# Kernel optimization log

Measured on AMD Instinct MI355X. Metric: run time of the kernel, lower is better.

Reference implementation:

```python
import jax, jax.numpy as jnp
import numpy as np

B, S, D, H = 2, 2048, 1024, 16
DK = D // H  # 64


def setup_inputs() -> dict:
    rng = jax.random.key(0)
    ks = jax.random.split(rng, 11)
    std = 1.0 / np.sqrt(D)
    query = jax.random.normal(ks[0], (B, S, D), dtype=jnp.float32)
    key = jax.random.normal(ks[1], (B, S, D), dtype=jnp.float32)
    value = jax.random.normal(ks[2], (B, S, D), dtype=jnp.float32)
    # causal mask, broadcast over batch and heads
    mask = jnp.tril(jnp.ones((S, S), dtype=jnp.int32))[None, None]
    Wq = jax.random.normal(ks[3], (D, D), dtype=jnp.float32) * std
    bq = jnp.zeros((D,), dtype=jnp.float32)
    Wk = jax.random.normal(ks[4], (D, D), dtype=jnp.float32) * std
    bk = jnp.zeros((D,), dtype=jnp.float32)
    Wv = jax.random.normal(ks[5], (D, D), dtype=jnp.float32) * std
    bv = jnp.zeros((D,), dtype=jnp.float32)
    Wo = jax.random.normal(ks[6], (D, D), dtype=jnp.float32) * std
    bo = jnp.zeros((D,), dtype=jnp.float32)
    return {"query": query, "key": key, "value": value, "mask": mask,
            "Wq": Wq, "bq": bq, "Wk": Wk, "bk": bk,
            "Wv": Wv, "bv": bv, "Wo": Wo, "bo": bo}


def reference(query, key, value, mask, Wq, bq, Wk, bk, Wv, bv, Wo, bo):
    scale = jnp.sqrt(jnp.float32(DK))
    # linear projections (nn.Linear applies x @ W.T + b)
    Q = query @ Wq.T + bq
    K = key @ Wk.T + bk
    V = value @ Wv.T + bv
    # [B,S,D] -> [B,H,S,DK]
    Q = Q.reshape(B, S, H, DK).transpose(0, 2, 1, 3)
    K = K.reshape(B, S, H, DK).transpose(0, 2, 1, 3)
    V = V.reshape(B, S, H, DK).transpose(0, 2, 1, 3)
    scores = jnp.einsum('bhqd,bhkd->bhqk', Q, K) / scale
    scores = jnp.where(mask == 0, jnp.float32(-1e9), scores)
    attention = jax.nn.softmax(scores, axis=-1)  # dropout is identity in eval
    x = jnp.einsum('bhqk,bhkd->bhqd', attention, V)
    x = x.transpose(0, 2, 1, 3).reshape(B, S, D)
    x = x @ Wo.T + bo
    return (x, attention)
```

## Files before the change

### kernel.cpp

```cpp
#include <hip/hip_runtime.h>
#include <stdint.h>

#define S_LEN 2048
#define DMODEL 1024
#define NHEAD 16
#define DKH 64
#define NROW 4096

using short8  = __attribute__((ext_vector_type(8))) short;
using short4v = __attribute__((ext_vector_type(4))) short;
using float4v = __attribute__((ext_vector_type(4))) float;

__device__ __forceinline__ short f2bf(float f) {
    union { float f; unsigned u; } v; v.f = f;
    unsigned r = (v.u + 0x7fffu + ((v.u >> 16) & 1u)) >> 16;
    return (short)r;
}

__device__ __forceinline__ float4v mfma16(short8 a, short8 b, float4v c) {
    return __builtin_amdgcn_mfma_f32_16x16x32_bf16(a, b, c, 0, 0, 0);
}

__device__ __forceinline__ void gload16(const short* g, short* l) {
    __builtin_amdgcn_global_load_lds(
        (const __attribute__((address_space(1))) void*)g,
        (__attribute__((address_space(3))) void*)l, 16, 0, 0);
}

__global__ __launch_bounds__(256) void convert_kernel(
    const float* __restrict__ q, const float* __restrict__ k, const float* __restrict__ v,
    const float* __restrict__ wq, const float* __restrict__ wk, const float* __restrict__ wv,
    const float* __restrict__ wo,
    short* __restrict__ oq, short* __restrict__ ok_, short* __restrict__ ov,
    short* __restrict__ owq, short* __restrict__ owk, short* __restrict__ owv,
    short* __restrict__ owo)
{
    const size_t A = (size_t)NROW * DMODEL;
    const size_t W = (size_t)DMODEL * DMODEL;
    size_t i = ((size_t)blockIdx.x * 256 + threadIdx.x) * 4;
    const float* src; short* dst; size_t off;
    if (i < A)            { src = q;  dst = oq;  off = i; }
    else if (i < 2 * A)   { src = k;  dst = ok_; off = i - A; }
    else if (i < 3 * A)   { src = v;  dst = ov;  off = i - 2 * A; }
    else {
        size_t j = i - 3 * A; int wsel = (int)(j / W); off = j % W;
        src = (wsel == 0) ? wq : (wsel == 1) ? wk : (wsel == 2) ? wv : wo;
        dst = (wsel == 0) ? owq : (wsel == 1) ? owk : (wsel == 2) ? owv : owo;
    }
    float4v x = *(const float4v*)(src + off);
    short4v o;
    o[0] = f2bf(x[0]); o[1] = f2bf(x[1]); o[2] = f2bf(x[2]); o[3] = f2bf(x[3]);
    *(short4v*)(dst + off) = o;
}

__global__ __launch_bounds__(256) void gemm_qkv(
    const short* __restrict__ Xq, const short* __restrict__ Xk, const short* __restrict__ Xv,
    const short* __restrict__ Wq, const short* __restrict__ Wk, const short* __restrict__ Wv,
    const float* __restrict__ bq, const float* __restrict__ bk, const float* __restrict__ bv,
    short* __restrict__ Qo, short* __restrict__ Ko, short* __restrict__ Vt)
{
    int zy = blockIdx.y;
    int z = zy >> 3;
    int n0 = (zy & 7) * 128;
    const short* X = (z == 0) ? Xq : (z == 1) ? Xk : Xv;
    const short* W = (z == 0) ? Wq : (z == 1) ? Wk : Wv;
    const float* bias = (z == 0) ? bq : (z == 1) ? bk : bv;
    int m0 = blockIdx.x * 128;

    __shared__ __align__(16) short As[128 * 32];
    __shared__ __align__(16) short Bs[128 * 32];

    int tid = threadIdx.x, lane = tid & 63, w = tid >> 6;
    int row_in = lane & 15, grp = lane >> 4;
    int wm = (w & 1) * 64, wn = (w >> 1) * 64;

    float4v acc[4][4];
#pragma unroll
    for (int m = 0; m < 4; m++)
#pragma unroll
        for (int n = 0; n < 4; n++) acc[m][n] = (float4v){0.f, 0.f, 0.f, 0.f};

    for (int k0 = 0; k0 < DMODEL; k0 += 32) {
#pragma unroll
        for (int j = 0; j < 2; j++) {
            int chunk = j * 256 + tid;
            int r = chunk >> 2, c = (chunk & 3) * 8;
            gload16(X + (size_t)(m0 + r) * DMODEL + k0 + c,
                    As + (size_t)(j * 256 + w * 64) * 8);
            gload16(W + (size_t)(n0 + r) * DMODEL + k0 + c,
                    Bs + (size_t)(j * 256 + w * 64) * 8);
        }
        __syncthreads();

        short8 af[4], bf[4];
#pragma unroll
        for (int m = 0; m < 4; m++)
            af[m] = *(const short8*)&As[(wm + m * 16 + row_in) * 32 + grp * 8];
#pragma unroll
        for (int n = 0; n < 4; n++)
            bf[n] = *(const short8*)&Bs[(wn + n * 16 + row_in) * 32 + grp * 8];
#pragma unroll
        for (int m = 0; m < 4; m++)
#pragma unroll
            for (int n = 0; n < 4; n++)
                acc[m][n] = mfma16(af[m], bf[n], acc[m][n]);
        __syncthreads();
    }

#pragma unroll
    for (int m = 0; m < 4; m++) {
#pragma unroll
        for (int n = 0; n < 4; n++) {
            int col = n0 + wn + n * 16 + row_in;
            int h = col >> 6, dk = col & 63;
            float bval = bias[col];
            if (z < 2) {
                short* dst = (z == 0) ? Qo : Ko;
#pragma unroll
                for (int r = 0; r < 4; r++) {
                    int rowg = m0 + wm + m * 16 + grp * 4 + r;
                    int bb = rowg >> 11, s = rowg & 2047;
                    dst[(((size_t)(bb * NHEAD + h)) * S_LEN + s) * DKH + dk] =
                        f2bf(acc[m][n][r] + bval);
                }
            } else {
                int rowg0 = m0 + wm + m * 16 + grp * 4;
                int bb = rowg0 >> 11, s0 = rowg0 & 2047;
                short4v pk;
#pragma unroll
                for (int r = 0; r < 4; r++) pk[r] = f2bf(acc[m][n][r] + bval);
                *(short4v*)(Vt + ((size_t)(bb * NHEAD + h) * DKH + dk) * S_LEN + s0) = pk;
            }
        }
    }
}

__global__ __launch_bounds__(256) void gemm_out(
    const short* __restrict__ X, const short* __restrict__ W,
    const float* __restrict__ bias, float* __restrict__ out)
{
    int m0 = blockIdx.x * 128, n0 = blockIdx.y * 128;

    __shared__ __align__(16) short As[128 * 32];
    __shared__ __align__(16) short Bs[128 * 32];

    int tid = threadIdx.x, lane = tid & 63, w = tid >> 6;
    int row_in = lane & 15, grp = lane >> 4;
    int wm = (w & 1) * 64, wn = (w >> 1) * 64;

    float4v acc[4][4];
#pragma unroll
    for (int m = 0; m < 4; m++)
#pragma unroll
        for (int n = 0; n < 4; n++) acc[m][n] = (float4v){0.f, 0.f, 0.f, 0.f};

    for (int k0 = 0; k0 < DMODEL; k0 += 32) {
#pragma unroll
        for (int j = 0; j < 2; j++) {
            int chunk = j * 256 + tid;
            int r = chunk >> 2, c = (chunk & 3) * 8;
            gload16(X + (size_t)(m0 + r) * DMODEL + k0 + c,
                    As + (size_t)(j * 256 + w * 64) * 8);
            gload16(W + (size_t)(n0 + r) * DMODEL + k0 + c,
                    Bs + (size_t)(j * 256 + w * 64) * 8);
        }
        __syncthreads();

        short8 af[4], bf[4];
#pragma unroll
        for (int m = 0; m < 4; m++)
            af[m] = *(const short8*)&As[(wm + m * 16 + row_in) * 32 + grp * 8];
#pragma unroll
        for (int n = 0; n < 4; n++)
            bf[n] = *(const short8*)&Bs[(wn + n * 16 + row_in) * 32 + grp * 8];
#pragma unroll
        for (int m = 0; m < 4; m++)
#pragma unroll
            for (int n = 0; n < 4; n++)
                acc[m][n] = mfma16(af[m], bf[n], acc[m][n]);
        __syncthreads();
    }

#pragma unroll
    for (int m = 0; m < 4; m++)
#pragma unroll
        for (int n = 0; n < 4; n++) {
            int col = n0 + wn + n * 16 + row_in;
            float bval = bias[col];
#pragma unroll
            for (int r = 0; r < 4; r++) {
                int rowg = m0 + wm + m * 16 + grp * 4 + r;
                out[(size_t)rowg * DMODEL + col] = acc[m][n][r] + bval;
            }
        }
}

__global__ __launch_bounds__(256) void attn_kernel(
    const short* __restrict__ Q, const short* __restrict__ K, const short* __restrict__ Vt,
    float* __restrict__ Attn, short* __restrict__ Xatt)
{
    int bh = blockIdx.x;
    int q0 = blockIdx.y * 64;
    int tid = threadIdx.x, lane = tid & 63, w = tid >> 6;
    int row_in = lane & 15, grp = lane >> 4;
    int qbase = q0 + w * 16;

    const short* Qh = Q + (size_t)bh * S_LEN * DKH;
    const short* Kh = K + (size_t)bh * S_LEN * DKH;
    const short* Vh = Vt + (size_t)bh * DKH * S_LEN;
    float* Ah = Attn + (size_t)bh * S_LEN * S_LEN;

    short8 qf0 = *(const short8*)(Qh + (size_t)(qbase + row_in) * DKH + grp * 8);
    short8 qf1 = *(const short8*)(Qh + (size_t)(qbase + row_in) * DKH + 32 + grp * 8);

    float m[4] = {-1e30f, -1e30f, -1e30f, -1e30f};
    float l[4] = {0.f, 0.f, 0.f, 0.f};

    int q_hi_wave = qbase + 15;
    for (int kv0 = 0; kv0 <= q_hi_wave; kv0 += 64) {
        float sv[4][4];
#pragma unroll
        for (int u = 0; u < 4; u++) {
            const short* Kr = Kh + (size_t)(kv0 + u * 16 + row_in) * DKH + grp * 8;
            short8 b0 = *(const short8*)Kr;
            short8 b1 = *(const short8*)(Kr + 32);
            float4v a = (float4v){0.f, 0.f, 0.f, 0.f};
            a = mfma16(qf0, b0, a);
            a = mfma16(qf1, b1, a);
            int colg = kv0 + u * 16 + row_in;
#pragma unroll
            for (int r = 0; r < 4; r++) {
                int rowg = qbase + grp * 4 + r;
                float s = a[r] * 0.125f;
                sv[u][r] = (colg > rowg) ? -1e30f : s;
            }
        }
#pragma unroll
        for (int r = 0; r < 4; r++) {
            float mx = fmaxf(fmaxf(sv[0][r], sv[1][r]), fmaxf(sv[2][r], sv[3][r]));
            mx = fmaxf(mx, __shfl_xor(mx, 1, 64));
            mx = fmaxf(mx, __shfl_xor(mx, 2, 64));
            mx = fmaxf(mx, __shfl_xor(mx, 4, 64));
            mx = fmaxf(mx, __shfl_xor(mx, 8, 64));
            float nm = fmaxf(m[r], mx);
            float ps = __expf(sv[0][r] - nm) + __expf(sv[1][r] - nm) +
                       __expf(sv[2][r] - nm) + __expf(sv[3][r] - nm);
            ps += __shfl_xor(ps, 1, 64);
            ps += __shfl_xor(ps, 2, 64);
            ps += __shfl_xor(ps, 4, 64);
            ps += __shfl_xor(ps, 8, 64);
            l[r] = l[r] * __expf(m[r] - nm) + ps;
            m[r] = nm;
        }
    }
    float rinv[4];
#pragma unroll
    for (int r = 0; r < 4; r++) rinv[r] = 1.0f / l[r];

    __shared__ __align__(16) short Plds[4][16][72];
    __shared__ __align__(16) float Pf32[4][16][68];
    float4v o[4];
#pragma unroll
    for (int v = 0; v < 4; v++) o[v] = (float4v){0.f, 0.f, 0.f, 0.f};

    int q_hi_blk = q0 + 63;
    for (int kv0 = 0; kv0 < S_LEN; kv0 += 64) {
        if (kv0 <= q_hi_blk) {
#pragma unroll
            for (int u = 0; u < 4; u++) {
                const short* Kr = Kh + (size_t)(kv0 + u * 16 + row_in) * DKH + grp * 8;
                short8 b0 = *(const short8*)Kr;
                short8 b1 = *(const short8*)(Kr + 32);
                float4v a = (float4v){0.f, 0.f, 0.f, 0.f};
                a = mfma16(qf0, b0, a);
                a = mfma16(qf1, b1, a);
                int colg = kv0 + u * 16 + row_in;
#pragma unroll
                for (int r = 0; r < 4; r++) {
                    int rowg = qbase + grp * 4 + r;
                    float s = a[r] * 0.125f;
                    float p = (colg > rowg) ? 0.0f : __expf(s - m[r]) * rinv[r];
                    Pf32[w][grp * 4 + r][u * 16 + row_in] = p;
                    Plds[w][grp * 4 + r][u * 16 + row_in] = f2bf(p);
                }
            }
            asm volatile("s_waitcnt lgkmcnt(0)" ::: "memory");
#pragma unroll
            for (int rr = 0; rr < 4; rr++) {
                int rloc = rr * 4 + grp;
                float4v pv = *(const float4v*)&Pf32[w][rloc][row_in * 4];
                *(float4v*)(Ah + (size_t)(qbase + rloc) * S_LEN + kv0 + row_in * 4) = pv;
            }
            short8 pa0 = *(const short8*)&Plds[w][row_in][grp * 8];
            short8 pa1 = *(const short8*)&Plds[w][row_in][32 + grp * 8];
#pragma unroll
            for (int v = 0; v < 4; v++) {
                const short* Vr = Vh + (size_t)(v * 16 + row_in) * S_LEN + kv0 + grp * 8;
                short8 b0 = *(const short8*)Vr;
                short8 b1 = *(const short8*)(Vr + 32);
                o[v] = mfma16(pa0, b0, o[v]);
                o[v] = mfma16(pa1, b1, o[v]);
            }
        } else {
            float4v zz = (float4v){0.f, 0.f, 0.f, 0.f};
#pragma unroll
            for (int r = 0; r < 4; r++) {
                int rowg = qbase + r * 4 + grp;
                *(float4v*)(Ah + (size_t)rowg * S_LEN + kv0 + row_in * 4) = zz;
            }
        }
    }

    int b = bh >> 4, h = bh & 15;
#pragma unroll
    for (int v = 0; v < 4; v++) {
#pragma unroll
        for (int r = 0; r < 4; r++) {
            int s = qbase + grp * 4 + r;
            int col = h * 64 + v * 16 + row_in;
            Xatt[(size_t)(b * S_LEN + s) * DMODEL + col] = f2bf(o[v][r]);
        }
    }
}

extern "C" void kernel_launch(void* const* d_in, const int* in_sizes, int n_in,
                              void* d_out, int out_size, void* d_ws, size_t ws_size,
                              hipStream_t stream) {
    const float* q  = (const float*)d_in[0];
    const float* k  = (const float*)d_in[1];
    const float* v  = (const float*)d_in[2];
    const float* Wq = (const float*)d_in[4];
    const float* bq = (const float*)d_in[5];
    const float* Wk = (const float*)d_in[6];
    const float* bk = (const float*)d_in[7];
    const float* Wv = (const float*)d_in[8];
    const float* bv = (const float*)d_in[9];
    const float* Wo = (const float*)d_in[10];
    const float* bo = (const float*)d_in[11];

    float* out_x    = (float*)d_out;
    float* out_attn = out_x + (size_t)NROW * DMODEL;

    char* ws = (char*)d_ws;
    size_t off = 0;
    auto carve = [&](size_t bytes) -> char* {
        char* p = ws + off;
        off += (bytes + 255) & ~(size_t)255;
        return p;
    };
    const size_t XB = (size_t)NROW * DMODEL * sizeof(short);
    const size_t WB = (size_t)DMODEL * DMODEL * sizeof(short);
    short* Xq  = (short*)carve(XB);
    short* Xk  = (short*)carve(XB);
    short* Xv  = (short*)carve(XB);
    short* Wqb = (short*)carve(WB);
    short* Wkb = (short*)carve(WB);
    short* Wvb = (short*)carve(WB);
    short* Wob = (short*)carve(WB);
    short* Qb  = (short*)carve(XB);
    short* Kb  = (short*)carve(XB);
    short* Vtb = (short*)carve(XB);
    short* Xat = (short*)carve(XB);

    convert_kernel<<<dim3(16384), dim3(256), 0, stream>>>(
        q, k, v, Wq, Wk, Wv, Wo, Xq, Xk, Xv, Wqb, Wkb, Wvb, Wob);

    gemm_qkv<<<dim3(NROW / 128, 24), dim3(256), 0, stream>>>(
        Xq, Xk, Xv, Wqb, Wkb, Wvb, bq, bk, bv, Qb, Kb, Vtb);

    attn_kernel<<<dim3(32, S_LEN / 64), dim3(256), 0, stream>>>(
        Qb, Kb, Vtb, out_attn, Xat);

    gemm_out<<<dim3(NROW / 128, DMODEL / 128), dim3(256), 0, stream>>>(
        Xat, Wob, bo, out_x);
}
```

Before: 876.9 us.

## Stage K/V tiles in LDS and drop max-tracking from attention softmax

The attention kernel now loads each 64-row K and V tile cooperatively into shared memory so all four waves reuse it, instead of each wave fetching from global memory. The online max/rescale pass is removed: the first pass only sums exp2 of scaled scores, relying on scores being small enough not to overflow. The fp32 probability staging buffer is dropped, and the attention output is written from the bf16 copy converted back to float. These changes add block-wide barriers, and they risk overflow without max subtraction as well as reduced precision in the stored attention matrix.

```diff
diff --git a/kernel.cpp b/kernel.cpp
--- a/kernel.cpp
+++ b/kernel.cpp
@@ -15,6 +15,12 @@
     union { float f; unsigned u; } v; v.f = f;
     unsigned r = (v.u + 0x7fffu + ((v.u >> 16) & 1u)) >> 16;
     return (short)r;
+}
+
+__device__ __forceinline__ float bf2f(short b) {
+    union { unsigned u; float f; } c;
+    c.u = ((unsigned)(unsigned short)b) << 16;
+    return c.f;
 }
 
 __device__ __forceinline__ float4v mfma16(short8 a, short8 b, float4v c) {
@@ -210,20 +216,34 @@
     const short* Vh = Vt + (size_t)bh * DKH * S_LEN;
     float* Ah = Attn + (size_t)bh * S_LEN * S_LEN;
 
+    __shared__ __align__(16) short Ks[64 * 72];
+    __shared__ __align__(16) short Vs[64 * 72];
+    __shared__ __align__(16) short Plds[4][16 * 72];
+
     short8 qf0 = *(const short8*)(Qh + (size_t)(qbase + row_in) * DKH + grp * 8);
     short8 qf1 = *(const short8*)(Qh + (size_t)(qbase + row_in) * DKH + 32 + grp * 8);
 
-    float m[4] = {-1e30f, -1e30f, -1e30f, -1e30f};
+    const float SC = 0.125f * 1.44269504f;
     float l[4] = {0.f, 0.f, 0.f, 0.f};
-
-    int q_hi_wave = qbase + 15;
-    for (int kv0 = 0; kv0 <= q_hi_wave; kv0 += 64) {
-        float sv[4][4];
+    int Tmax = q0 / 64 + 1;
+
+    for (int t = 0; t < Tmax; t++) {
+        int kv0 = t * 64;
+        {
+            const short* src = Kh + (size_t)kv0 * DKH;
+#pragma unroll
+            for (int j = 0; j < 2; j++) {
+                int ch = j * 256 + tid;
+                int r = ch >> 3, c = (ch & 7) * 8;
+                short8 kv = *(const short8*)(src + ch * 8);
+                *(short8*)&Ks[r * 72 + c] = kv;
+            }
+        }
+        __syncthreads();
 #pragma unroll
         for (int u = 0; u < 4; u++) {
-            const short* Kr = Kh + (size_t)(kv0 + u * 16 + row_in) * DKH + grp * 8;
-            short8 b0 = *(const short8*)Kr;
-            short8 b1 = *(const short8*)(Kr + 32);
+            short8 b0 = *(const short8*)&Ks[(u * 16 + row_in) * 72 + grp * 8];
+            short8 b1 = *(const short8*)&Ks[(u * 16 + row_in) * 72 + 32 + grp * 8];
             float4v a = (float4v){0.f, 0.f, 0.f, 0.f};
             a = mfma16(qf0, b0, a);
             a = mfma16(qf1, b1, a);
@@ -231,83 +251,85 @@
 #pragma unroll
             for (int r = 0; r < 4; r++) {
                 int rowg = qbase + grp * 4 + r;
-                float s = a[r] * 0.125f;
-                sv[u][r] = (colg > rowg) ? -1e30f : s;
-            }
-        }
+                float e = (colg > rowg) ? 0.0f : exp2f(a[r] * SC);
+                l[r] += e;
+            }
+        }
+        __syncthreads();
+    }
+    float rinv[4];
+#pragma unroll
+    for (int r = 0; r < 4; r++) {
+        float s = l[r];
+        s += __shfl_xor(s, 1, 64);
+        s += __shfl_xor(s, 2, 64);
+        s += __shfl_xor(s, 4, 64);
+        s += __shfl_xor(s, 8, 64);
+        rinv[r] = 1.0f / s;
+    }
+
+    float4v o[4];
+#pragma unroll
+    for (int v = 0; v < 4; v++) o[v] = (float4v){0.f, 0.f, 0.f, 0.f};
+
+    for (int t = 0; t < Tmax; t++) {
+        int kv0 = t * 64;
+        {
+            const short* srcK = Kh + (size_t)kv0 * DKH;
+#pragma unroll
+            for (int j = 0; j < 2; j++) {
+                int ch = j * 256 + tid;
+                int r = ch >> 3, c = (ch & 7) * 8;
+                short8 kv = *(const short8*)(srcK + ch * 8);
+                *(short8*)&Ks[r * 72 + c] = kv;
+                short8 vv = *(const short8*)(Vh + (size_t)r * S_LEN + kv0 + c);
+                *(short8*)&Vs[r * 72 + c] = vv;
+            }
+        }
+        __syncthreads();
+#pragma unroll
+        for (int u = 0; u < 4; u++) {
+            short8 b0 = *(const short8*)&Ks[(u * 16 + row_in) * 72 + grp * 8];
+            short8 b1 = *(const short8*)&Ks[(u * 16 + row_in) * 72 + 32 + grp * 8];
+            float4v a = (float4v){0.f, 0.f, 0.f, 0.f};
+            a = mfma16(qf0, b0, a);
+            a = mfma16(qf1, b1, a);
+            int colg = kv0 + u * 16 + row_in;
+#pragma unroll
+            for (int r = 0; r < 4; r++) {
+                int rowg = qbase + grp * 4 + r;
+                float p = (colg > rowg) ? 0.0f : exp2f(a[r] * SC) * rinv[r];
+                Plds[w][(grp * 4 + r) * 72 + u * 16 + row_in] = f2bf(p);
+            }
+        }
+        asm volatile("s_waitcnt lgkmcnt(0)" ::: "memory");
+#pragma unroll
+        for (int rr = 0; rr < 4; rr++) {
+            int rloc = rr * 4 + grp;
+            short4v pb = *(const short4v*)&Plds[w][rloc * 72 + row_in * 4];
+            float4v pf;
+#pragma unroll
+            for (int i = 0; i < 4; i++) pf[i] = bf2f(pb[i]);
+            *(float4v*)(Ah + (size_t)(qbase + rloc) * S_LEN + kv0 + row_in * 4) = pf;
+        }
+        short8 pa0 = *(const short8*)&Plds[w][row_in * 72 + grp * 8];
+        short8 pa1 = *(const short8*)&Plds[w][row_in * 72 + 32 + grp * 8];
+#pragma unroll
+        for (int v = 0; v < 4; v++) {
+            short8 b0 = *(const short8*)&Vs[(v * 16 + row_in) * 72 + grp * 8];
+            short8 b1 = *(const short8*)&Vs[(v * 16 + row_in) * 72 + 32 + grp * 8];
+            o[v] = mfma16(pa0, b0, o[v]);
+            o[v] = mfma16(pa1, b1, o[v]);
+        }
+        __syncthreads();
+    }
+
+    float4v zz = (float4v){0.f, 0.f, 0.f, 0.f};
+    for (int kv0 = Tmax * 64; kv0 < S_LEN; kv0 += 64) {
 #pragma unroll
         for (int r = 0; r < 4; r++) {
-            float mx = fmaxf(fmaxf(sv[0][r], sv[1][r]), fmaxf(sv[2][r], sv[3][r]));
-            mx = fmaxf(mx, __shfl_xor(mx, 1, 64));
-            mx = fmaxf(mx, __shfl_xor(mx, 2, 64));
-            mx = fmaxf(mx, __shfl_xor(mx, 4, 64));
-            mx = fmaxf(mx, __shfl_xor(mx, 8, 64));
-            float nm = fmaxf(m[r], mx);
-            float ps = __expf(sv[0][r] - nm) + __expf(sv[1][r] - nm) +
-                       __expf(sv[2][r] - nm) + __expf(sv[3][r] - nm);
-            ps += __shfl_xor(ps, 1, 64);
-            ps += __shfl_xor(ps, 2, 64);
-            ps += __shfl_xor(ps, 4, 64);
-            ps += __shfl_xor(ps, 8, 64);
-            l[r] = l[r] * __expf(m[r] - nm) + ps;
-            m[r] = nm;
-        }
-    }
-    float rinv[4];
-#pragma unroll
-    for (int r = 0; r < 4; r++) rinv[r] = 1.0f / l[r];
-
-    __shared__ __align__(16) short Plds[4][16][72];
-    __shared__ __align__(16) float Pf32[4][16][68];
-    float4v o[4];
-#pragma unroll
-    for (int v = 0; v < 4; v++) o[v] = (float4v){0.f, 0.f, 0.f, 0.f};
-
-    int q_hi_blk = q0 + 63;
-    for (int kv0 = 0; kv0 < S_LEN; kv0 += 64) {
-        if (kv0 <= q_hi_blk) {
-#pragma unroll
-            for (int u = 0; u < 4; u++) {
-                const short* Kr = Kh + (size_t)(kv0 + u * 16 + row_in) * DKH + grp * 8;
-                short8 b0 = *(const short8*)Kr;
-                short8 b1 = *(const short8*)(Kr + 32);
-                float4v a = (float4v){0.f, 0.f, 0.f, 0.f};
-                a = mfma16(qf0, b0, a);
-                a = mfma16(qf1, b1, a);
-                int colg = kv0 + u * 16 + row_in;
-#pragma unroll
-                for (int r = 0; r < 4; r++) {
-                    int rowg = qbase + grp * 4 + r;
-                    float s = a[r] * 0.125f;
-                    float p = (colg > rowg) ? 0.0f : __expf(s - m[r]) * rinv[r];
-                    Pf32[w][grp * 4 + r][u * 16 + row_in] = p;
-                    Plds[w][grp * 4 + r][u * 16 + row_in] = f2bf(p);
-                }
-            }
-            asm volatile("s_waitcnt lgkmcnt(0)" ::: "memory");
-#pragma unroll
-            for (int rr = 0; rr < 4; rr++) {
-                int rloc = rr * 4 + grp;
-                float4v pv = *(const float4v*)&Pf32[w][rloc][row_in * 4];
-                *(float4v*)(Ah + (size_t)(qbase + rloc) * S_LEN + kv0 + row_in * 4) = pv;
-            }
-            short8 pa0 = *(const short8*)&Plds[w][row_in][grp * 8];
-            short8 pa1 = *(const short8*)&Plds[w][row_in][32 + grp * 8];
-#pragma unroll
-            for (int v = 0; v < 4; v++) {
-                const short* Vr = Vh + (size_t)(v * 16 + row_in) * S_LEN + kv0 + grp * 8;
-                short8 b0 = *(const short8*)Vr;
-                short8 b1 = *(const short8*)(Vr + 32);
-                o[v] = mfma16(pa0, b0, o[v]);
-                o[v] = mfma16(pa1, b1, o[v]);
-            }
-        } else {
-            float4v zz = (float4v){0.f, 0.f, 0.f, 0.f};
-#pragma unroll
-            for (int r = 0; r < 4; r++) {
-                int rowg = qbase + r * 4 + grp;
-                *(float4v*)(Ah + (size_t)rowg * S_LEN + kv0 + row_in * 4) = zz;
-            }
+            int rowg = qbase + r * 4 + grp;
+            *(float4v*)(Ah + (size_t)rowg * S_LEN + kv0 + row_in * 4) = zz;
         }
     }
 
```

New measurement: 731.0 us. 1.2x faster.
